# Performance work log

Measured on AMD Instinct MI355X. Metric: run time of the kernel, lower is better.

## Reference

```python
import jax, jax.numpy as jnp
import numpy as np

B, A, C = 64, 8732, 81


def setup_inputs() -> dict:
    key = jax.random.key(0)
    k1, k2, k3, k4, k5 = jax.random.split(key, 5)
    scores = jax.random.normal(k1, (B, A, C), dtype=jnp.float32)
    boxes = jax.random.normal(k2, (B, A, 4), dtype=jnp.float32)
    gt_labels = jax.random.randint(k3, (B, A), 0, C)
    gt_boxes = jax.random.normal(k4, (B, A, 4), dtype=jnp.float32)
    mask = jax.random.uniform(k5, (B, A)) < 0.02
    return {"scores": scores, "boxes": boxes, "gt_labels": gt_labels,
            "gt_boxes": gt_boxes, "mask": mask}


def reference(scores, boxes, gt_labels, gt_boxes, mask):
    dtype = scores.dtype
    maskf = mask.astype(dtype)
    pos_num = mask.sum(axis=-1, keepdims=True)          # [B,1] per-image positives
    N = jnp.maximum(1, mask.sum()).astype(dtype)        # max(1, total positives)

    # localization: smooth L1 (beta=1) summed over positive anchors
    d = boxes - gt_boxes
    ad = jnp.abs(d)
    sl1 = jnp.where(ad < 1.0, 0.5 * d * d, ad - 0.5)    # [B,A,4]
    loc_loss = (sl1.sum(axis=-1) * maskf).sum() / N

    # per-anchor cross entropy
    logp = jax.nn.log_softmax(scores, axis=-1)          # [B,A,C]
    c_loss = -jnp.take_along_axis(logp, gt_labels[..., None], axis=-1)[..., 0]  # [B,A]

    # hard negative mining: zero positives, rank by descending loss, keep top 3*pos_num
    conf_neg = jnp.where(mask, jnp.zeros((), dtype), c_loss)
    conf_idx = jnp.argsort(-conf_neg, axis=-1)          # descending sort indices
    rank = jnp.argsort(conf_idx, axis=-1)               # rank of each anchor
    neg_mask = rank < 3 * pos_num                       # [B,A]

    conf_loss = ((c_loss * maskf).sum() + (c_loss * neg_mask.astype(dtype)).sum()) / N
    total_loss = loc_loss + conf_loss
    return total_loss, loc_loss, conf_loss
```

## Files before the change

### kernel.cpp

```cpp
#include <hip/hip_runtime.h>
#include <hip/hip_bf16.h>
#include <math.h>

#define NB 64
#define NA 8732
#define NC 81
#define TOTAL (NB * NA)
#define APB 128
#define TPB 512
#define NBLK (TOTAL / APB)


__global__ void init_kernel(int* __restrict__ pos_count, float* __restrict__ acc) {
    const int t = threadIdx.x;
    if (t < NB) pos_count[t] = 0;
    else if (t < NB + 3) acc[t - NB] = 0.0f;
}

__device__ __forceinline__ float quadsum(float x) {
    x += __int_as_float(__builtin_amdgcn_update_dpp(
        0, __float_as_int(x), 0xB1, 0xF, 0xF, true));
    x += __int_as_float(__builtin_amdgcn_update_dpp(
        0, __float_as_int(x), 0x4E, 0xF, 0xF, true));
    return x;
}

__global__ __launch_bounds__(TPB) void main_kernel(
    const float* __restrict__ scores, const float* __restrict__ boxes,
    const int* __restrict__ gt_labels, const float* __restrict__ gt_boxes,
    const int* __restrict__ mask, float* __restrict__ conf_neg,
    int* __restrict__ pos_count, float* __restrict__ block_loc,
    float* __restrict__ block_pcs)
{
    __shared__ float lds[APB * NC];
    __shared__ float wredl[8], wredp[8];
    __shared__ int posc[2];
    const int tid  = threadIdx.x;
    const int lane = tid & 63;
    const int wid  = tid >> 6;
    const int base = blockIdx.x * APB;
    const int b0   = base / NA;

    if (tid < 2) posc[tid] = 0;
    __syncthreads();

    const float4* __restrict__ src = (const float4*)(scores + (size_t)base * NC);
    float4* dst = (float4*)lds;
    const float4 t0 = src[tid];
    const float4 t1 = src[tid + 512];
    const float4 t2 = src[tid + 1024];
    const float4 t3 = src[tid + 1536];
    const float4 t4 = src[tid + 2048];
    float4 t5;
    if (tid < 32) t5 = src[tid + 2560];
    dst[tid] = t0; dst[tid + 512] = t1; dst[tid + 1024] = t2;
    dst[tid + 1536] = t3; dst[tid + 2048] = t4;
    if (tid < 32) dst[tid + 2560] = t5;

    float loc = 0.0f;
    if (tid < APB) {
        const int a = base + tid;
        if (mask[a]) {
            const float4 bx = *(const float4*)(boxes    + (size_t)a * 4);
            const float4 gb = *(const float4*)(gt_boxes + (size_t)a * 4);
            const float d0 = bx.x - gb.x, d1 = bx.y - gb.y;
            const float d2 = bx.z - gb.z, d3 = bx.w - gb.w;
            const float a0 = fabsf(d0), a1 = fabsf(d1), a2 = fabsf(d2), a3 = fabsf(d3);
            loc = (a0 < 1.f ? 0.5f * d0 * d0 : a0 - 0.5f)
                + (a1 < 1.f ? 0.5f * d1 * d1 : a1 - 0.5f)
                + (a2 < 1.f ? 0.5f * d2 * d2 : a2 - 0.5f)
                + (a3 < 1.f ? 0.5f * d3 * d3 : a3 - 0.5f);
            atomicAdd(&posc[(a / NA) - b0], 1);
        }
    }
    __syncthreads();

    const int al = tid >> 2;
    const int q  = tid & 3;
    const float* __restrict__ row = lds + al * NC;
    float e = 0.0f;
    #pragma unroll
    for (int j = 0; j < 20; ++j) e += __expf(row[q * 20 + j]);
    if (q == 3) e += __expf(row[80]);
    e = quadsum(e);

    float pcs = 0.0f;
    if (q == 0) {
        const int a = base + al;
        const int lab = gt_labels[a];
        const float c = __logf(e) - row[lab];
        const int m = mask[a];
        conf_neg[a] = m ? 0.f : c;
        pcs = m ? c : 0.f;
    }

    #pragma unroll
    for (int o = 32; o; o >>= 1) {
        loc += __shfl_down(loc, o);
        pcs += __shfl_down(pcs, o);
    }
    if (lane == 0) { wredl[wid] = loc; wredp[wid] = pcs; }
    __syncthreads();
    if (tid == 0) {
        float sl = 0.f, sp = 0.f;
        #pragma unroll
        for (int w = 0; w < 8; ++w) { sl += wredl[w]; sp += wredp[w]; }
        block_loc[blockIdx.x] = sl;
        block_pcs[blockIdx.x] = sp;
    }
    if (tid < 2 && posc[tid] > 0)
        atomicAdd(&pos_count[b0 + tid], posc[tid]);
}

__global__ __launch_bounds__(1024) void topk_kernel(
    const float* __restrict__ conf_neg, const int* __restrict__ pos_count,
    float* __restrict__ acc)
{
    __shared__ unsigned sv[NA];
    __shared__ int whist[16][256];
    __shared__ int hist[256];
    __shared__ int   redi[16];
    __shared__ float redf[16];
    __shared__ unsigned spfx;
    __shared__ int skr;
    const int tid = threadIdx.x;
    const int wid = tid >> 6;
    const int b = blockIdx.x;
    const float* __restrict__ row = conf_neg + (size_t)b * NA;

    for (int i = tid; i < NA; i += 1024) sv[i] = __float_as_uint(row[i]);

    int k = 3 * pos_count[b];
    if (k <= 0) return;
    if (k > NA) k = NA;
    __syncthreads();

    unsigned prefix = 0u;
    int kr = k;
    for (int shift = 24; shift >= 0; shift -= 8) {
        #pragma unroll
        for (int j = tid; j < 16 * 256; j += 1024) ((int*)whist)[j] = 0;
        __syncthreads();
        const unsigned himask = (shift == 24) ? 0u : (0xFFFFFFFFu << (shift + 8));
        for (int i = tid; i < NA; i += 1024) {
            const unsigned v = sv[i];
            if ((v & himask) == prefix)
                atomicAdd(&whist[wid][(v >> shift) & 255], 1);
        }
        __syncthreads();
        if (tid < 256) {
            int s = 0;
            #pragma unroll
            for (int w = 0; w < 16; ++w) s += whist[w][tid];
            hist[tid] = s;
        }
        __syncthreads();
        for (int off = 1; off < 256; off <<= 1) {
            int val = 0;
            if (tid < 256) val = hist[tid] + ((tid + off < 256) ? hist[tid + off] : 0);
            __syncthreads();
            if (tid < 256) hist[tid] = val;
            __syncthreads();
        }
        if (tid < 256) {
            const int sj  = hist[tid];
            const int sj1 = (tid < 255) ? hist[tid + 1] : 0;
            if (sj >= kr && sj1 < kr) {
                spfx = prefix | ((unsigned)tid << shift);
                skr  = kr - sj1;
            }
        }
        __syncthreads();
        prefix = spfx;
        kr = skr;
        __syncthreads();
    }
    float s = 0.0f; int cg = 0;
    for (int i = tid; i < NA; i += 1024) {
        const unsigned u = sv[i];
        if (u > prefix) { s += __uint_as_float(u); cg++; }
    }
    #pragma unroll
    for (int o = 32; o; o >>= 1) { s += __shfl_down(s, o); cg += __shfl_down(cg, o); }
    if ((tid & 63) == 0) { redf[wid] = s; redi[wid] = cg; }
    __syncthreads();
    if (tid == 0) {
        float ts = 0.f; int tc = 0;
        #pragma unroll
        for (int w = 0; w < 16; ++w) { ts += redf[w]; tc += redi[w]; }
        ts += (float)(k - tc) * __uint_as_float(prefix);
        atomicAdd(&acc[2], ts);
    }
}

__global__ __launch_bounds__(1024) void final_kernel(
    const float* __restrict__ block_loc, const float* __restrict__ block_pcs,
    const int* __restrict__ pos_count, const float* __restrict__ acc,
    float* __restrict__ out)
{
    __shared__ float rl[16], rp[16];
    const int tid = threadIdx.x;
    const int wid = tid >> 6;
    float sl = 0.f, sp = 0.f;
    for (int i = tid; i < NBLK; i += 1024) { sl += block_loc[i]; sp += block_pcs[i]; }
    int p = (tid < NB) ? pos_count[tid] : 0;
    #pragma unroll
    for (int o = 32; o; o >>= 1) {
        sl += __shfl_down(sl, o);
        sp += __shfl_down(sp, o);
        p  += __shfl_down(p, o);
    }
    if ((tid & 63) == 0) { rl[wid] = sl; rp[wid] = sp; }
    __syncthreads();
    if (tid == 0) {
        float tl = 0.f, tp = 0.f;
        #pragma unroll
        for (int w = 0; w < 16; ++w) { tl += rl[w]; tp += rp[w]; }
        const float N = fmaxf(1.0f, (float)p);
        const float loc  = tl / N;
        const float conf = (tp + acc[2]) / N;
        out[0] = loc + conf;
        out[1] = loc;
        out[2] = conf;
    }
}

extern "C" void kernel_launch(void* const* d_in, const int* in_sizes, int n_in,
                              void* d_out, int out_size, void* d_ws, size_t ws_size,
                              hipStream_t stream) {
    const float* scores    = (const float*)d_in[0];
    const float* boxes     = (const float*)d_in[1];
    const int*   gt_labels = (const int*)d_in[2];
    const float* gt_boxes  = (const float*)d_in[3];
    const int*   mask      = (const int*)d_in[4];
    float* out = (float*)d_out;

    float* conf_neg  = (float*)d_ws;
    int*   pos_count = (int*)(conf_neg + TOTAL);
    float* acc       = (float*)(pos_count + NB);
    float* block_loc = acc + 3;
    float* block_pcs = block_loc + NBLK;

    hipLaunchKernelGGL(init_kernel, dim3(1), dim3(128), 0, stream, pos_count, acc);
    hipLaunchKernelGGL(main_kernel, dim3(NBLK), dim3(TPB), 0, stream,
                       scores, boxes, gt_labels, gt_boxes, mask,
                       conf_neg, pos_count, block_loc, block_pcs);
    hipLaunchKernelGGL(topk_kernel, dim3(NB), dim3(1024), 0, stream,
                       conf_neg, pos_count, acc);
    hipLaunchKernelGGL(final_kernel, dim3(1), dim3(1024), 0, stream,
                       block_loc, block_pcs, pos_count, acc, out);
}
```

Measured before the change: 292.5 us.

## Speed up radix select with finer histogram privatization and wave-level scan

Replaces the barrier-heavy shared-memory suffix scan in the per-image radix select with a single-wavefront shuffle scan over 4 bins per lane. Histograms are privatized per 16 threads instead of per wave to reduce LDS atomic contention, and they are zeroed with vector stores and reduced in two stages using all threads. One redundant barrier per pass is removed, and blocks with no positives return before loading the row. This costs more LDS (64x256 ints), which may limit occupancy, but only 64 blocks run anyway.

```diff
diff --git a/kernel.cpp b/kernel.cpp
--- a/kernel.cpp
+++ b/kernel.cpp
@@ -117,64 +117,80 @@
     float* __restrict__ acc)
 {
     __shared__ unsigned sv[NA];
-    __shared__ int whist[16][256];
-    __shared__ int hist[256];
+    __shared__ __align__(16) int whist[64][256];
+    __shared__ int hist4[4][256];
     __shared__ int   redi[16];
     __shared__ float redf[16];
     __shared__ unsigned spfx;
     __shared__ int skr;
-    const int tid = threadIdx.x;
-    const int wid = tid >> 6;
+    const int tid  = threadIdx.x;
+    const int lane = tid & 63;
+    const int wid  = tid >> 6;
+    const int hid  = tid >> 4;
     const int b = blockIdx.x;
     const float* __restrict__ row = conf_neg + (size_t)b * NA;
-
-    for (int i = tid; i < NA; i += 1024) sv[i] = __float_as_uint(row[i]);
 
     int k = 3 * pos_count[b];
     if (k <= 0) return;
     if (k > NA) k = NA;
+
+    for (int i = tid; i < NA; i += 1024) sv[i] = __float_as_uint(row[i]);
     __syncthreads();
 
     unsigned prefix = 0u;
     int kr = k;
     for (int shift = 24; shift >= 0; shift -= 8) {
-        #pragma unroll
-        for (int j = tid; j < 16 * 256; j += 1024) ((int*)whist)[j] = 0;
-        __syncthreads();
+        int4* w4 = (int4*)whist;
+        const int4 z = make_int4(0, 0, 0, 0);
+        w4[tid] = z; w4[tid + 1024] = z; w4[tid + 2048] = z; w4[tid + 3072] = z;
+        __syncthreads();
+
         const unsigned himask = (shift == 24) ? 0u : (0xFFFFFFFFu << (shift + 8));
         for (int i = tid; i < NA; i += 1024) {
             const unsigned v = sv[i];
             if ((v & himask) == prefix)
-                atomicAdd(&whist[wid][(v >> shift) & 255], 1);
-        }
-        __syncthreads();
-        if (tid < 256) {
+                atomicAdd(&whist[hid][(v >> shift) & 255], 1);
+        }
+        __syncthreads();
+
+        {
+            const int p = tid >> 8;
+            const int bb = tid & 255;
             int s = 0;
             #pragma unroll
-            for (int w = 0; w < 16; ++w) s += whist[w][tid];
-            hist[tid] = s;
-        }
-        __syncthreads();
-        for (int off = 1; off < 256; off <<= 1) {
-            int val = 0;
-            if (tid < 256) val = hist[tid] + ((tid + off < 256) ? hist[tid + off] : 0);
-            __syncthreads();
-            if (tid < 256) hist[tid] = val;
-            __syncthreads();
-        }
-        if (tid < 256) {
-            const int sj  = hist[tid];
-            const int sj1 = (tid < 255) ? hist[tid + 1] : 0;
-            if (sj >= kr && sj1 < kr) {
-                spfx = prefix | ((unsigned)tid << shift);
-                skr  = kr - sj1;
+            for (int w = 0; w < 16; ++w) s += whist[(p << 4) + w][bb];
+            hist4[p][bb] = s;
+        }
+        __syncthreads();
+
+        if (wid == 0) {
+            int h0, h1, h2, h3;
+            {
+                const int b0i = 4 * lane;
+                h0 = hist4[0][b0i]     + hist4[1][b0i]     + hist4[2][b0i]     + hist4[3][b0i];
+                h1 = hist4[0][b0i + 1] + hist4[1][b0i + 1] + hist4[2][b0i + 1] + hist4[3][b0i + 1];
+                h2 = hist4[0][b0i + 2] + hist4[1][b0i + 2] + hist4[2][b0i + 2] + hist4[3][b0i + 2];
+                h3 = hist4[0][b0i + 3] + hist4[1][b0i + 3] + hist4[2][b0i + 3] + hist4[3][b0i + 3];
             }
+            const int s3 = h3, s2 = h2 + s3, s1 = h1 + s2, s0 = h0 + s1;
+            int incl = s0;
+            #pragma unroll
+            for (int off = 1; off < 64; off <<= 1) {
+                const int v = __shfl_down(incl, off);
+                if (lane + off < 64) incl += v;
+            }
+            const int E = incl - s0;
+            const int S0 = E + s0, S1 = E + s1, S2 = E + s2, S3 = E + s3;
+            if (S0 >= kr && S1 < kr) { spfx = prefix | ((unsigned)(4 * lane)     << shift); skr = kr - S1; }
+            else if (S1 >= kr && S2 < kr) { spfx = prefix | ((unsigned)(4 * lane + 1) << shift); skr = kr - S2; }
+            else if (S2 >= kr && S3 < kr) { spfx = prefix | ((unsigned)(4 * lane + 2) << shift); skr = kr - S3; }
+            else if (S3 >= kr && E  < kr) { spfx = prefix | ((unsigned)(4 * lane + 3) << shift); skr = kr - E;  }
         }
         __syncthreads();
         prefix = spfx;
         kr = skr;
-        __syncthreads();
-    }
+    }
+
     float s = 0.0f; int cg = 0;
     for (int i = tid; i < NA; i += 1024) {
         const unsigned u = sv[i];
```

After: 292.1 us. No clear change (-0.2%).
